# Optimization experiments

Hardware: AMD Instinct MI355X
Metric: run time of the kernel (lower is better)

The kernel has to match this reference:

```python
import jax, jax.numpy as jnp
import numpy as np

B, H, N, P = 2, 8, 2048, 64   # batch, heads, seq, head_dim
M, D = 4, 256                 # sketch count, sketch feature dim


def setup_inputs() -> dict:
    key = jax.random.key(0)
    kq, kk, ks, kr = jax.random.split(key, 4)
    scale = P ** -0.5  # keep exp(QK) numerically tame, std(dot) ~= 1/8
    Q = jax.random.normal(kq, (B, H, N, P), dtype=jnp.float32) * scale
    K = jax.random.normal(kk, (B, H, N, P), dtype=jnp.float32) * scale
    # indices into the concatenated [Q;K] token axis of length 2N
    sketching_matrix = jax.random.randint(ks, (B, M, D), 0, 2 * N)
    # Rademacher random signs, broadcast over [b,h,2n] in the reduction
    random_sign = jnp.sign(jax.random.normal(kr, (M, D), dtype=jnp.float32))
    random_sign = jnp.where(random_sign == 0, 1.0, random_sign)
    return {"Q": Q, "K": K, "sketching_matrix": sketching_matrix,
            "random_sign": random_sign}


def reference(Q, K, sketching_matrix, random_sign):
    b, h, n, p = Q.shape
    X = jnp.concatenate([Q, K], axis=2)          # [b,h,2n,p]
    Xt = jnp.transpose(X, (0, 2, 1, 3))          # [b,2n,h,p]
    # gather sketched landmarks: [b,m,d,h,p] -> [b,h,m,d,p]
    XS = Xt[jnp.arange(b)[:, None, None], sketching_matrix]
    XS = jnp.transpose(XS, (0, 3, 1, 2, 4))
    # RS_SM accumulate branch: exp of inner products, random-sign reduce over m
    product = jnp.einsum('bhnp,bhmdp->bhnmd', X, XS)   # [b,h,2n,m,d]
    AS = jnp.einsum('bhnmd,md->bhnd', jnp.exp(product), random_sign)
    return AS.astype(Q.dtype)                    # [b,h,2n,d]
```

## Files before the change

kernel.cpp:

```cpp
#include <hip/hip_runtime.h>
#include <hip/hip_bf16.h>

typedef __attribute__((ext_vector_type(8))) short short8;
typedef __attribute__((ext_vector_type(4))) float f32x4;

namespace {
constexpr int Nc  = 2048;
constexpr int NXc = 4096;
constexpr int Pc  = 64;
constexpr int Mc  = 4;
constexpr int Dc  = 256;
constexpr int BH  = 16;
constexpr float LOG2E = 1.4426950408889634f;
}

__device__ inline float fexp2(float x) {
#if __has_builtin(__builtin_amdgcn_exp2f)
  return __builtin_amdgcn_exp2f(x);
#else
  return exp2f(x);
#endif
}

__device__ inline unsigned int bfpack(float a, float b) {
  union { __hip_bfloat162 h; unsigned int u; } cv;
  cv.h = __float22bfloat162_rn(make_float2(a, b));
  return cv.u;
}

__global__ __launch_bounds__(256, 4) void sketch_fused(
    const float* __restrict__ Q, const float* __restrict__ K,
    const int* __restrict__ SK, const float* __restrict__ SGN,
    float* __restrict__ OUT)
{
  __shared__ __hip_bfloat16 Ws[Mc * 64 * Pc];

  const int t    = threadIdx.x;
  const int lane = t & 63;
  const int wv   = t >> 6;
  const int brow = lane & 15;
  const int q    = lane >> 4;
  const int bh   = blockIdx.y;
  const int b    = bh >> 3;

  const int bx  = blockIdx.x;
  const int xcd = bx & 7;
  const int rr  = bx >> 3;
  const int nch = xcd * 4 + (rr >> 2);
  const int dq  = rr & 3;
  const int n0  = nch * 128;
  const int d0  = dq * 64;

  char* wsb = (char*)Ws;

  {
    const int dl = t >> 2;
    const int qt = t & 3;
    const int* skp = SK + b * (Mc * Dc) + d0 + dl;
    const int sw = (dl & 7) << 4;
    #pragma unroll
    for (int m = 0; m < 4; ++m) {
      const int idx = skp[m * Dc];
      const float* src = ((idx < Nc) ? (Q + ((size_t)bh * Nc + idx) * Pc)
                                     : (K + ((size_t)bh * Nc + (idx - Nc)) * Pc))
                         + qt * 16;
      f32x4 f0 = *(const f32x4*)(src);
      f32x4 f1 = *(const f32x4*)(src + 4);
      f32x4 f2 = *(const f32x4*)(src + 8);
      f32x4 f3 = *(const f32x4*)(src + 12);
      uint4 ua, ub;
      ua.x = bfpack(f0.x * LOG2E, f0.y * LOG2E);
      ua.y = bfpack(f0.z * LOG2E, f0.w * LOG2E);
      ua.z = bfpack(f1.x * LOG2E, f1.y * LOG2E);
      ua.w = bfpack(f1.z * LOG2E, f1.w * LOG2E);
      ub.x = bfpack(f2.x * LOG2E, f2.y * LOG2E);
      ub.y = bfpack(f2.z * LOG2E, f2.w * LOG2E);
      ub.z = bfpack(f3.x * LOG2E, f3.y * LOG2E);
      ub.w = bfpack(f3.z * LOG2E, f3.w * LOG2E);
      char* rp = wsb + (m * 64 + dl) * 128;
      *(uint4*)(rp + ((qt * 32) ^ sw))      = ua;
      *(uint4*)(rp + ((qt * 32 + 16) ^ sw)) = ub;
    }
  }
  __syncthreads();

  const int swr = (brow & 7) << 4;
  #pragma unroll
  for (int tt = 0; tt < 2; ++tt) {
    const int it = wv * 2 + tt;
    const int nr = n0 + it * 16 + brow;
    const float* xp = ((n0 < Nc) ? (Q + ((size_t)bh * Nc + nr) * Pc)
                                 : (K + ((size_t)bh * Nc + (nr - Nc)) * Pc))
                      + q * 8;
    f32x4 x0 = *(const f32x4*)(xp);
    f32x4 x1 = *(const f32x4*)(xp + 4);
    f32x4 x2 = *(const f32x4*)(xp + 32);
    f32x4 x3 = *(const f32x4*)(xp + 36);
    short8 b0, b1;
    {
      union { short8 s; uint4 u; } c0, c1;
      c0.u.x = bfpack(x0.x, x0.y); c0.u.y = bfpack(x0.z, x0.w);
      c0.u.z = bfpack(x1.x, x1.y); c0.u.w = bfpack(x1.z, x1.w);
      c1.u.x = bfpack(x2.x, x2.y); c1.u.y = bfpack(x2.z, x2.w);
      c1.u.z = bfpack(x3.x, x3.y); c1.u.w = bfpack(x3.z, x3.w);
      b0 = c0.s; b1 = c1.s;
    }

    float* orow = OUT + ((size_t)bh * NXc + nr) * Dc + d0 + q * 4;
    #pragma unroll
    for (int dt = 0; dt < 4; ++dt) {
      f32x4 acc = {0.f, 0.f, 0.f, 0.f};
      #pragma unroll
      for (int m = 0; m < 4; ++m) {
        const char* ap = wsb + (m * 64 + dt * 16 + brow) * 128;
        short8 a0 = *(const short8*)(ap + ((q * 16) ^ swr));
        short8 a1 = *(const short8*)(ap + ((64 + q * 16) ^ swr));
        f32x4 c = {0.f, 0.f, 0.f, 0.f};
        c = __builtin_amdgcn_mfma_f32_16x16x32_bf16(a0, b0, c, 0, 0, 0);
        c = __builtin_amdgcn_mfma_f32_16x16x32_bf16(a1, b1, c, 0, 0, 0);
        const f32x4 sg = *(const f32x4*)(SGN + m * Dc + d0 + dt * 16 + q * 4);
        acc.x = fmaf(sg.x, fexp2(c.x), acc.x);
        acc.y = fmaf(sg.y, fexp2(c.y), acc.y);
        acc.z = fmaf(sg.z, fexp2(c.z), acc.z);
        acc.w = fmaf(sg.w, fexp2(c.w), acc.w);
      }
      *(f32x4*)(orow + dt * 16) = acc;
    }
  }
}

extern "C" void kernel_launch(void* const* d_in, const int* in_sizes, int n_in,
                              void* d_out, int out_size, void* d_ws, size_t ws_size,
                              hipStream_t stream) {
  (void)in_sizes; (void)n_in; (void)out_size; (void)d_ws; (void)ws_size;
  const float* Q   = (const float*)d_in[0];
  const float* K   = (const float*)d_in[1];
  const int*   SK  = (const int*)d_in[2];
  const float* SGN = (const float*)d_in[3];
  float* OUT = (float*)d_out;

  sketch_fused<<<dim3(128, BH), dim3(256), 0, stream>>>(Q, K, SK, SGN, OUT);
}
```

Measured before the change: 109.2 us.

## Double rows per block and reuse each LDS sketch fragment across four row tiles

Each block now covers 256 rows instead of 128, and the grid is halved to 64 blocks along x. Each wave loads four 16-row X tiles into registers and reuses every LDS A fragment and sign load across all four MFMA tiles. This halves the number of times the sketch landmarks are gathered, converted and written to LDS, and cuts LDS reads per output. The cost is higher register pressure (four accumulators plus eight B fragments) and half as many blocks, which may lower occupancy and latency hiding.

```diff
diff --git a/kernel.cpp b/kernel.cpp
--- a/kernel.cpp
+++ b/kernel.cpp
@@ -46,9 +46,9 @@
   const int bx  = blockIdx.x;
   const int xcd = bx & 7;
   const int rr  = bx >> 3;
-  const int nch = xcd * 4 + (rr >> 2);
+  const int nch = xcd * 2 + (rr >> 2);
   const int dq  = rr & 3;
-  const int n0  = nch * 128;
+  const int n0  = nch * 256;
   const int d0  = dq * 64;
 
   char* wsb = (char*)Ws;
@@ -84,47 +84,55 @@
   }
   __syncthreads();
 
-  const int swr = (brow & 7) << 4;
+  const float* xr = ((n0 < Nc) ? (Q + ((size_t)bh * Nc + n0) * Pc)
+                               : (K + ((size_t)bh * Nc + (n0 - Nc)) * Pc))
+                    + (size_t)(wv * 64 + brow) * Pc + q * 8;
+  short8 b0[4], b1[4];
   #pragma unroll
-  for (int tt = 0; tt < 2; ++tt) {
-    const int it = wv * 2 + tt;
-    const int nr = n0 + it * 16 + brow;
-    const float* xp = ((n0 < Nc) ? (Q + ((size_t)bh * Nc + nr) * Pc)
-                                 : (K + ((size_t)bh * Nc + (nr - Nc)) * Pc))
-                      + q * 8;
+  for (int tt = 0; tt < 4; ++tt) {
+    const float* xp = xr + (size_t)tt * 16 * Pc;
     f32x4 x0 = *(const f32x4*)(xp);
     f32x4 x1 = *(const f32x4*)(xp + 4);
     f32x4 x2 = *(const f32x4*)(xp + 32);
     f32x4 x3 = *(const f32x4*)(xp + 36);
-    short8 b0, b1;
-    {
-      union { short8 s; uint4 u; } c0, c1;
-      c0.u.x = bfpack(x0.x, x0.y); c0.u.y = bfpack(x0.z, x0.w);
-      c0.u.z = bfpack(x1.x, x1.y); c0.u.w = bfpack(x1.z, x1.w);
-      c1.u.x = bfpack(x2.x, x2.y); c1.u.y = bfpack(x2.z, x2.w);
-      c1.u.z = bfpack(x3.x, x3.y); c1.u.w = bfpack(x3.z, x3.w);
-      b0 = c0.s; b1 = c1.s;
+    union { short8 s; uint4 u; } c0, c1;
+    c0.u.x = bfpack(x0.x, x0.y); c0.u.y = bfpack(x0.z, x0.w);
+    c0.u.z = bfpack(x1.x, x1.y); c0.u.w = bfpack(x1.z, x1.w);
+    c1.u.x = bfpack(x2.x, x2.y); c1.u.y = bfpack(x2.z, x2.w);
+    c1.u.z = bfpack(x3.x, x3.y); c1.u.w = bfpack(x3.z, x3.w);
+    b0[tt] = c0.s; b1[tt] = c1.s;
+  }
+
+  const int swr = (brow & 7) << 4;
+  float* obase = OUT + ((size_t)bh * NXc + n0 + wv * 64 + brow) * Dc + d0 + q * 4;
+
+  #pragma unroll
+  for (int dt = 0; dt < 4; ++dt) {
+    f32x4 acc[4];
+    #pragma unroll
+    for (int tt = 0; tt < 4; ++tt) acc[tt] = (f32x4){0.f, 0.f, 0.f, 0.f};
+
+    #pragma unroll
+    for (int m = 0; m < 4; ++m) {
+      const char* ap = wsb + (m * 64 + dt * 16 + brow) * 128;
+      short8 a0 = *(const short8*)(ap + ((q * 16) ^ swr));
+      short8 a1 = *(const short8*)(ap + ((64 + q * 16) ^ swr));
+      const f32x4 sg = *(const f32x4*)(SGN + m * Dc + d0 + dt * 16 + q * 4);
+      #pragma unroll
+      for (int tt = 0; tt < 4; ++tt) {
+        f32x4 c = {0.f, 0.f, 0.f, 0.f};
+        c = __builtin_amdgcn_mfma_f32_16x16x32_bf16(a0, b0[tt], c, 0, 0, 0);
+        c = __builtin_amdgcn_mfma_f32_16x16x32_bf16(a1, b1[tt], c, 0, 0, 0);
+        acc[tt].x = fmaf(sg.x, fexp2(c.x), acc[tt].x);
+        acc[tt].y = fmaf(sg.y, fexp2(c.y), acc[tt].y);
+        acc[tt].z = fmaf(sg.z, fexp2(c.z), acc[tt].z);
+        acc[tt].w = fmaf(sg.w, fexp2(c.w), acc[tt].w);
+      }
     }
 
-    float* orow = OUT + ((size_t)bh * NXc + nr) * Dc + d0 + q * 4;
     #pragma unroll
-    for (int dt = 0; dt < 4; ++dt) {
-      f32x4 acc = {0.f, 0.f, 0.f, 0.f};
-      #pragma unroll
-      for (int m = 0; m < 4; ++m) {
-        const char* ap = wsb + (m * 64 + dt * 16 + brow) * 128;
-        short8 a0 = *(const short8*)(ap + ((q * 16) ^ swr));
-        short8 a1 = *(const short8*)(ap + ((64 + q * 16) ^ swr));
-        f32x4 c = {0.f, 0.f, 0.f, 0.f};
-        c = __builtin_amdgcn_mfma_f32_16x16x32_bf16(a0, b0, c, 0, 0, 0);
-        c = __builtin_amdgcn_mfma_f32_16x16x32_bf16(a1, b1, c, 0, 0, 0);
-        const f32x4 sg = *(const f32x4*)(SGN + m * Dc + d0 + dt * 16 + q * 4);
-        acc.x = fmaf(sg.x, fexp2(c.x), acc.x);
-        acc.y = fmaf(sg.y, fexp2(c.y), acc.y);
-        acc.z = fmaf(sg.z, fexp2(c.z), acc.z);
-        acc.w = fmaf(sg.w, fexp2(c.w), acc.w);
-      }
-      *(f32x4*)(orow + dt * 16) = acc;
+    for (int tt = 0; tt < 4; ++tt) {
+      *(f32x4*)(obase + (size_t)tt * 16 * Dc + dt * 16) = acc[tt];
     }
   }
 }
@@ -139,5 +147,5 @@
   const float* SGN = (const float*)d_in[3];
   float* OUT = (float*)d_out;
 
-  sketch_fused<<<dim3(128, BH), dim3(256), 0, stream>>>(Q, K, SK, SGN, OUT);
+  sketch_fused<<<dim3(64, BH), dim3(256), 0, stream>>>(Q, K, SK, SGN, OUT);
 }
```

Measured after the change: 104.5 us. 4.3% less time.
